# Kernel optimization log

Hardware: AMD Instinct MI355X
Metric: run time of the kernel (lower is better)

Reference implementation:

```python
import jax, jax.numpy as jnp
import numpy as np

DIM = 4096
N_HEADS = 32
N_KV_HEADS = 8
HEAD_DIM = DIM // N_HEADS  # 128
N_REP = N_HEADS // N_KV_HEADS  # 4
THETA = 10000.0
B, S = 4, 1024


def setup_inputs() -> dict:
    key = jax.random.key(0)
    ks = jax.random.split(key, 5)
    sc = 1.0 / np.sqrt(DIM).astype(np.float32)
    x = jax.random.normal(ks[0], (B, S, DIM), jnp.float32)
    wq = jax.random.normal(ks[1], (DIM, N_HEADS * HEAD_DIM), jnp.float32) * sc
    wk = jax.random.normal(ks[2], (DIM, N_KV_HEADS * HEAD_DIM), jnp.float32) * sc
    wv = jax.random.normal(ks[3], (DIM, N_KV_HEADS * HEAD_DIM), jnp.float32) * sc
    wo = jax.random.normal(ks[4], (N_HEADS * HEAD_DIM, DIM), jnp.float32) * sc
    return {"x": x, "wq": wq, "wk": wk, "wv": wv, "wo": wo}


def _rope_cos_sin(seq_len):
    # matches precompute_freqs_cis: freqs over even indices, angles = t * freqs
    freqs = 1.0 / (THETA ** (jnp.arange(0, HEAD_DIM, 2, dtype=jnp.float32) / HEAD_DIM))
    t = jnp.arange(seq_len, dtype=jnp.float32)
    ang = jnp.outer(t, freqs)  # [S, HEAD_DIM//2]
    return jnp.cos(ang), jnp.sin(ang)


def _apply_rope(x, cos, sin):
    # x: [B, S, H, D]; consecutive pairs form complex numbers (view_as_complex)
    xr = x[..., 0::2]
    xi = x[..., 1::2]
    c = cos[None, :, None, :]
    s = sin[None, :, None, :]
    out_r = xr * c - xi * s
    out_i = xr * s + xi * c
    return jnp.stack([out_r, out_i], axis=-1).reshape(x.shape)


def reference(x, wq, wk, wv, wo):
    bsz, seq_len, _ = x.shape
    q = (x @ wq).reshape(bsz, seq_len, N_HEADS, HEAD_DIM)
    k = (x @ wk).reshape(bsz, seq_len, N_KV_HEADS, HEAD_DIM)
    v = (x @ wv).reshape(bsz, seq_len, N_KV_HEADS, HEAD_DIM)
    cos, sin = _rope_cos_sin(seq_len)
    q = _apply_rope(q, cos, sin)
    k = _apply_rope(k, cos, sin)
    # repeat_kv: expand each kv head N_REP times contiguously
    k = jnp.repeat(k, N_REP, axis=2)
    v = jnp.repeat(v, N_REP, axis=2)
    scores = jnp.einsum('bqhd,bkhd->bhqk', q, k) / np.float32(np.sqrt(HEAD_DIM))
    mask = jnp.triu(jnp.full((seq_len, seq_len), -jnp.inf, dtype=scores.dtype), k=1)
    scores = scores + mask
    attn = jax.nn.softmax(scores.astype(jnp.float32), axis=-1).astype(q.dtype)
    out = jnp.einsum('bhqk,bkhd->bqhd', attn, v).reshape(bsz, seq_len, N_HEADS * HEAD_DIM)
    return out @ wo
```

## Files before the change

### kernel.cpp

```cpp
#include <hip/hip_runtime.h>

typedef unsigned short u16;
typedef unsigned int u32;
typedef __attribute__((ext_vector_type(8))) short short8_t;
typedef __attribute__((ext_vector_type(4))) float f32x4;

static constexpr int Bc = 4, Sc = 1024, Hc = 32, HKVc = 8, Dc = 128;
static constexpr int BS = Bc * Sc;
static constexpr int DIMc = 4096;

__device__ __forceinline__ u16 f2bf(float f) {
  u32 u = __float_as_uint(f);
  u32 r = (u + 0x7fffu + ((u >> 16) & 1u)) >> 16;
  return (u16)r;
}
__device__ __forceinline__ float bf2f(u16 u) {
  return __uint_as_float(((u32)u) << 16);
}
__device__ __forceinline__ void gload_lds16(const void* g, void* l) {
  __builtin_amdgcn_global_load_lds((const __attribute__((address_space(1))) void*)g,
                                   (__attribute__((address_space(3))) void*)l, 16, 0, 0);
}

#define SBAR __builtin_amdgcn_sched_barrier(0)
#define PBARRIER do { SBAR; __builtin_amdgcn_s_barrier(); SBAR; } while (0)
#define WAITVM(N) asm volatile("s_waitcnt vmcnt(" #N ")" ::: "memory")

__global__ void rope_table_k(float* __restrict__ tbl) {
  int i = blockIdx.x * 256 + threadIdx.x;
  int s = i >> 6, fi = i & 63;
  float freq = powf(10000.f, -(float)fi / 64.f);
  float ang = (float)s * freq;
  float sv, cv;
  sincosf(ang, &sv, &cv);
  tbl[2 * i] = cv;
  tbl[2 * i + 1] = sv;
}

__global__ void f32_to_bf16_k(const float* __restrict__ in, u16* __restrict__ out, int n4) {
  int i = blockIdx.x * 256 + threadIdx.x;
  if (i >= n4) return;
  float4 v = *(const float4*)(in + (size_t)i * 4);
  uint2 pk;
  pk.x = (u32)f2bf(v.x) | ((u32)f2bf(v.y) << 16);
  pk.y = (u32)f2bf(v.z) | ((u32)f2bf(v.w) << 16);
  *(uint2*)(out + (size_t)i * 4) = pk;
}

__global__ __launch_bounds__(256) void transpose_w_k(const float* __restrict__ W, u16* __restrict__ WT,
                                                     int Kdim, int Ndim) {
  __shared__ float tile[64 * 65];
  const int t = threadIdx.x;
  const int n0 = blockIdx.x * 64, k0 = blockIdx.y * 64;
  #pragma unroll
  for (int p = 0; p < 4; ++p) {
    int idx = p * 256 + t;
    int r = idx >> 4, c = (idx & 15) * 4;
    float4 v = *(const float4*)(W + (size_t)(k0 + r) * Ndim + n0 + c);
    tile[r * 65 + c + 0] = v.x;
    tile[r * 65 + c + 1] = v.y;
    tile[r * 65 + c + 2] = v.z;
    tile[r * 65 + c + 3] = v.w;
  }
  __syncthreads();
  #pragma unroll
  for (int p = 0; p < 2; ++p) {
    int idx = p * 256 + t;
    int n = idx >> 3, c = (idx & 7) * 8;
    alignas(16) u16 o[8];
    #pragma unroll
    for (int i = 0; i < 8; ++i) o[i] = f2bf(tile[(c + i) * 65 + n]);
    *(uint4*)(WT + (size_t)(n0 + n) * Kdim + k0 + c) = *(const uint4*)o;
  }
}

#define MFMAQ(QI)                                                                        \
  do {                                                                                   \
    __builtin_amdgcn_s_setprio(1);                                                       \
    _Pragma("unroll") for (int mf = 0; mf < 4; ++mf)                                     \
      _Pragma("unroll") for (int nf = 0; nf < 2; ++nf)                                   \
        _Pragma("unroll") for (int kk = 0; kk < 2; ++kk)                                 \
          acc[QI][mf][nf] = __builtin_amdgcn_mfma_f32_16x16x32_bf16(                     \
              af[mf][kk], bf[nf][kk], acc[QI][mf][nf], 0, 0, 0);                         \
    __builtin_amdgcn_s_setprio(0);                                                       \
  } while (0)

template <int MODE>
__global__ __launch_bounds__(512, 2) void gemm256(const u16* __restrict__ A, const u16* __restrict__ BT,
                                                  void* __restrict__ Cv, const float* __restrict__ tbl,
                                                  int M, int N, int K) {
  extern __shared__ char smem[];
  const int t = threadIdx.x, l = t & 63, w = t >> 6;
  const int ln15 = l & 15, lh = l >> 4;
  const int NT = K >> 6;

  int id = blockIdx.x;
  int nwg = gridDim.x;
  int swz = ((nwg & 7) == 0) ? ((id & 7) * (nwg >> 3) + (id >> 3)) : id;
  const int nbn = N >> 8;
  const int bm = swz / nbn, bn = swz % nbn;

  const u16* Ag = A + (size_t)bm * 256 * K;
  const u16* Bg = BT + (size_t)bn * 256 * K;

  f32x4 acc[4][4][2];
  #pragma unroll
  for (int q = 0; q < 4; ++q)
    #pragma unroll
    for (int mf = 0; mf < 4; ++mf)
      #pragma unroll
      for (int nf = 0; nf < 2; ++nf) acc[q][mf][nf] = f32x4{0.f, 0.f, 0.f, 0.f};
  short8_t af[4][2], bf[2][2];

  const int srow = (l >> 3);
  const int sck  = (l & 7) ^ srow;
  auto stageA = [&](char* bufbase, int h, int tt) {
    char* lb = bufbase + h * 16384 + w * 1024;
    const u16* g = Ag + (size_t)(h * 128 + w * 8 + srow) * K + tt * 64 + (sck << 3);
    gload_lds16(g, lb);
    gload_lds16(g + (size_t)64 * K, lb + 8192);
  };
  auto stageB = [&](char* bufbase, int h, int tt) {
    char* lb = bufbase + 32768 + h * 16384 + w * 1024;
    const u16* g = Bg + (size_t)(h * 128 + w * 8 + srow) * K + tt * 64 + (sck << 3);
    gload_lds16(g, lb);
    gload_lds16(g + (size_t)64 * K, lb + 8192);
  };
  const int arow = (w >> 2) * 64 + ln15;
  const int brow = (w & 3) * 32 + ln15;
  const int rsw = ln15 & 7;
  auto LDA = [&](const char* cb, int qm) {
    #pragma unroll
    for (int mf = 0; mf < 4; ++mf)
      #pragma unroll
      for (int kk = 0; kk < 2; ++kk)
        af[mf][kk] = *(const short8_t*)(cb + qm * 16384 + (arow + mf * 16) * 128 +
                                        (((kk * 4 + lh) ^ rsw) << 4));
  };
  auto LDB = [&](const char* cb, int qn) {
    #pragma unroll
    for (int nf = 0; nf < 2; ++nf)
      #pragma unroll
      for (int kk = 0; kk < 2; ++kk)
        bf[nf][kk] = *(const short8_t*)(cb + 32768 + qn * 16384 + (brow + nf * 16) * 128 +
                                        (((kk * 4 + lh) ^ rsw) << 4));
  };

  {
    char* b0 = smem;
    char* b1 = smem + 65536;
    stageB(b0, 0, 0);
    stageA(b0, 1, 0);
    stageA(b0, 0, 0);
    stageB(b0, 1, 0);
    stageB(b1, 0, 1);
    stageA(b1, 1, 1);
    stageB(b1, 1, 1);
  }
  WAITVM(6);
  PBARRIER;

  for (int T = 0; T < NT; ++T) {
    char* cb = smem + (T & 1) * 65536;
    char* nb = smem + ((T & 1) ^ 1) * 65536;
    const bool s1 = (T + 1 < NT), s2 = (T + 2 < NT);
    LDA(cb, 0); LDB(cb, 0);
    if (s1) stageA(nb, 0, T + 1);
    MFMAQ(0);
    PBARRIER;
    LDA(cb, 1);
    if (s2) stageB(cb, 0, T + 2);
    MFMAQ(1);
    PBARRIER;
    LDB(cb, 1);
    if (s2) stageA(cb, 1, T + 2);
    MFMAQ(2);
    PBARRIER;
    LDA(cb, 0);
    if (s2) stageB(cb, 1, T + 2);
    MFMAQ(3);
    if (s2)      { WAITVM(6); }
    else if (s1) { WAITVM(0); }
    PBARRIER;
  }

  const int rw = (w >> 2) * 64, cw = (w & 3) * 32;
  #pragma unroll
  for (int qi = 0; qi < 4; ++qi) {
    const int qm = (qi == 1 || qi == 2) ? 1 : 0;
    const int qn = (qi >= 2) ? 1 : 0;
    #pragma unroll
    for (int mf = 0; mf < 4; ++mf)
      #pragma unroll
      for (int nf = 0; nf < 2; ++nf)
        #pragma unroll
        for (int e = 0; e < 4; ++e) {
          int row = bm * 256 + qm * 128 + rw + mf * 16 + lh * 4 + e;
          int col = bn * 256 + qn * 128 + cw + nf * 16 + ln15;
          float v = acc[qi][mf][nf][e];
          if (MODE == 2) {
            float pv = __shfl_xor(v, 1);
            int d = col & 127, hh = col >> 7;
            int s = row & (Sc - 1), bb = row >> 10;
            float2 cs = *(const float2*)(tbl + (size_t)(s * 64 + (d >> 1)) * 2);
            float o = (d & 1) ? (v * cs.x + pv * cs.y) : (v * cs.x - pv * cs.y);
            o *= 0.08838834764831845f;
            ((u16*)Cv)[(((size_t)(bb * Hc + hh) * Sc + s) << 7) + d] = f2bf(o);
          } else {
            size_t idx = (size_t)row * N + col;
            ((float*)Cv)[idx] = v;
          }
        }
  }
}

#define MFMAKV(QM)                                                                       \
  do {                                                                                   \
    __builtin_amdgcn_s_setprio(1);                                                       \
    _Pragma("unroll") for (int mf = 0; mf < 4; ++mf)                                     \
      _Pragma("unroll") for (int nf = 0; nf < 2; ++nf)                                   \
        _Pragma("unroll") for (int kk = 0; kk < 2; ++kk)                                 \
          acc[QM][mf][nf] = __builtin_amdgcn_mfma_f32_16x16x32_bf16(                     \
              af[mf][kk], bf[nf][kk], acc[QM][mf][nf], 0, 0, 0);                         \
    __builtin_amdgcn_s_setprio(0);                                                       \
  } while (0)

__global__ __launch_bounds__(512, 1) void gemm_kv(const u16* __restrict__ A, const u16* __restrict__ BT,
                                                  u16* __restrict__ Krp, u16* __restrict__ Vtp,
                                                  const float* __restrict__ tbl) {
  extern __shared__ char smem[];
  const int t = threadIdx.x, l = t & 63, w = t >> 6;
  const int ln15 = l & 15, lh = l >> 4;
  const int K = 4096, NT = 64;

  int id = blockIdx.x;
  int swz = (id & 7) * 32 + (id >> 3);
  const int bm = swz >> 4, bn = swz & 15;

  const u16* Ag = A + (size_t)bm * 256 * K;
  const u16* Bg = BT + (size_t)bn * 128 * K;

  f32x4 acc[2][4][2];
  #pragma unroll
  for (int q = 0; q < 2; ++q)
    #pragma unroll
    for (int mf = 0; mf < 4; ++mf)
      #pragma unroll
      for (int nf = 0; nf < 2; ++nf) acc[q][mf][nf] = f32x4{0.f, 0.f, 0.f, 0.f};
  short8_t af[4][2], bf[2][2];

  const int srow = (l >> 3);
  const int sck  = (l & 7) ^ srow;
  auto stageA = [&](int buf, int h, int tt) {
    char* lb = smem + buf * 32768 + h * 16384 + w * 2048;
    const u16* g = Ag + (size_t)(h * 128 + w * 16 + srow) * K + tt * 64 + (sck << 3);
    gload_lds16(g, lb);
    gload_lds16(g + (size_t)8 * K, lb + 1024);
  };
  auto stageB = [&](int buf, int tt) {
    char* lb = smem + 65536 + buf * 16384 + w * 2048;
    const u16* g = Bg + (size_t)(w * 16 + srow) * K + tt * 64 + (sck << 3);
    gload_lds16(g, lb);
    gload_lds16(g + (size_t)8 * K, lb + 1024);
  };
  const int arow = (w >> 2) * 64 + ln15;
  const int brow = (w & 3) * 32 + ln15;
  const int rsw = ln15 & 7;
  auto LDA = [&](int buf, int qm) {
    #pragma unroll
    for (int mf = 0; mf < 4; ++mf)
      #pragma unroll
      for (int kk = 0; kk < 2; ++kk)
        af[mf][kk] = *(const short8_t*)(smem + buf * 32768 + qm * 16384 + (arow + mf * 16) * 128 +
                                        (((kk * 4 + lh) ^ rsw) << 4));
  };
  auto LDB = [&](int buf) {
    #pragma unroll
    for (int nf = 0; nf < 2; ++nf)
      #pragma unroll
      for (int kk = 0; kk < 2; ++kk)
        bf[nf][kk] = *(const short8_t*)(smem + 65536 + buf * 16384 + (brow + nf * 16) * 128 +
                                        (((kk * 4 + lh) ^ rsw) << 4));
  };

  stageA(0, 0, 0);
  stageB(0, 0);
  stageA(0, 1, 0);
  WAITVM(2);
  PBARRIER;

  for (int T = 0; T < NT; ++T) {
    const int cb = T & 1, nb = cb ^ 1;
    const bool st = (T + 1 < NT);
    LDA(cb, 0); LDB(cb);
    if (st) stageA(nb, 0, T + 1);
    MFMAKV(0);
    if (st) { WAITVM(2); } else { WAITVM(0); }
    PBARRIER;
    LDA(cb, 1);
    if (st) { stageB(nb, T + 1); stageA(nb, 1, T + 1); }
    MFMAKV(1);
    if (st) { WAITVM(2); }
    PBARRIER;
  }

  #pragma unroll
  for (int qm = 0; qm < 2; ++qm)
    #pragma unroll
    for (int mf = 0; mf < 4; ++mf)
      #pragma unroll
      for (int nf = 0; nf < 2; ++nf)
        #pragma unroll
        for (int e = 0; e < 4; ++e) {
          int row = bm * 256 + qm * 128 + (w >> 2) * 64 + mf * 16 + lh * 4 + e;
          int col = bn * 128 + (w & 3) * 32 + nf * 16 + ln15;
          float v = acc[qm][mf][nf][e];
          float pv = __shfl_xor(v, 1);
          int s = row & (Sc - 1), bb = row >> 10;
          if (col < 1024) {
            int hkv = col >> 7, d = col & 127;
            float2 cs = *(const float2*)(tbl + (size_t)(s * 64 + (d >> 1)) * 2);
            float o = (d & 1) ? (v * cs.x + pv * cs.y) : (v * cs.x - pv * cs.y);
            Krp[(((size_t)(bb * HKVc + hkv) * Sc + s) << 7) + d] = f2bf(o);
          } else {
            int vc = col - 1024;
            int hkv = vc >> 7, d = vc & 127;
            int sl = s & 63;
            int sg = (sl & 32) | (((sl >> 2) & 3) << 3) | (((sl >> 4) & 1) << 2) | (sl & 3);
            Vtp[((size_t)(bb * HKVc + hkv) * Dc + d) * Sc + (s & ~63) + sg] = f2bf(v);
          }
        }
}

__global__ __launch_bounds__(512, 4) void attn_k(const u16* __restrict__ Q, const u16* __restrict__ Kr,
                                                 const u16* __restrict__ Vt, u16* __restrict__ AO) {
  extern __shared__ char smem[];
  const int t = threadIdx.x, l = t & 63, w = t >> 6;
  const int qb = (int)gridDim.x - 1 - (int)blockIdx.x;
  const int h = blockIdx.y, b = blockIdx.z;
  const int hkv = h >> 2;
  const int ln15 = l & 15, lh = l >> 4;
  const int NT = 2 * qb + 2;

  const u16* Kg0 = Kr + (size_t)(b * HKVc + hkv) * Sc * Dc;
  const u16* Vg0 = Vt + (size_t)(b * HKVc + hkv) * Dc * Sc;

  auto stageK = [&](int buf, int tt) {
    char* base = smem + buf * 16384 + w * 2048;
    #pragma unroll
    for (int i = 0; i < 2; ++i) {
      int row = w * 8 + i * 4 + (l >> 4);
      int c = l & 15;
      gload_lds16(Kg0 + (size_t)(tt * 64 + row) * Dc + ((c ^ (row & 7)) << 3), base + i * 1024);
    }
  };
  auto stageV = [&](int buf, int tt) {
    char* base = smem + 32768 + buf * 16384 + w * 2048;
    #pragma unroll
    for (int i = 0; i < 2; ++i) {
      int d = w * 16 + i * 8 + (l >> 3);
      int c = l & 7;
      gload_lds16(Vg0 + (size_t)d * Sc + tt * 64 + ((c ^ (d & 7)) << 3), base + i * 1024);
    }
  };

  short8_t qf[4];
  {
    int q = qb * 128 + w * 16 + ln15;
    const u16* qp = Q + ((size_t)(b * Hc + h) * Sc + q) * Dc + lh * 8;
    #pragma unroll
    for (int ks = 0; ks < 4; ++ks) qf[ks] = *(const short8_t*)(qp + ks * 32);
  }
  SBAR;

  f32x4 oacc[8];
  #pragma unroll
  for (int i = 0; i < 8; ++i) oacc[i] = f32x4{0.f, 0.f, 0.f, 0.f};
  float mrun = -1e30f, lrun = 0.f;

  stageK(0, 0); stageV(0, 0);
  stageK(1, 1); stageV(1, 1);

  const int qmaxw = qb * 128 + w * 16 + 15;
  const int qlane = qb * 128 + w * 16 + ln15;

  for (int T = 0; T < NT; ++T) {
    if (T < NT - 1) { WAITVM(4); } else { WAITVM(0); }
    PBARRIER;
    const char* Kb = smem + (T & 1) * 16384;
    const char* Vb = smem + 32768 + (T & 1) * 16384;

    if (T * 64 <= qmaxw) {
      f32x4 sf[4];
      #pragma unroll
      for (int fc = 0; fc < 4; ++fc) {
        sf[fc] = f32x4{0.f, 0.f, 0.f, 0.f};
        int kvr = fc * 16 + ln15;
        #pragma unroll
        for (int ks = 0; ks < 4; ++ks) {
          int chunk = ks * 4 + lh;
          short8_t kf = *(const short8_t*)(Kb + kvr * 256 + ((chunk ^ (kvr & 7)) << 4));
          sf[fc] = __builtin_amdgcn_mfma_f32_16x16x32_bf16(kf, qf[ks], sf[fc], 0, 0, 0);
        }
      }
      if (T * 64 + 63 > qb * 128 + w * 16) {
        #pragma unroll
        for (int fc = 0; fc < 4; ++fc)
          #pragma unroll
          for (int j = 0; j < 4; ++j) {
            int kvg = T * 64 + fc * 16 + lh * 4 + j;
            if (kvg > qlane) sf[fc][j] = -1e30f;
          }
      }
      float mx = sf[0][0];
      #pragma unroll
      for (int fc = 0; fc < 4; ++fc)
        #pragma unroll
        for (int j = 0; j < 4; ++j) mx = fmaxf(mx, sf[fc][j]);
      mx = fmaxf(mx, __shfl_xor(mx, 16));
      mx = fmaxf(mx, __shfl_xor(mx, 32));
      float mnew = fmaxf(mrun, mx);
      float alpha = __expf(mrun - mnew);
      mrun = mnew;
      float rs = 0.f;
      #pragma unroll
      for (int fc = 0; fc < 4; ++fc)
        #pragma unroll
        for (int j = 0; j < 4; ++j) {
          float p = __expf(sf[fc][j] - mnew);
          sf[fc][j] = p;
          rs += p;
        }
      rs += __shfl_xor(rs, 16);
      rs += __shfl_xor(rs, 32);
      lrun = lrun * alpha + rs;
      float arow[4];
      #pragma unroll
      for (int j = 0; j < 4; ++j) arow[j] = __shfl(alpha, (l & 48) | (lh * 4 + j));
      #pragma unroll
      for (int fd = 0; fd < 8; ++fd)
        #pragma unroll
        for (int j = 0; j < 4; ++j) oacc[fd][j] *= arow[j];
      short8_t pa[2];
      #pragma unroll
      for (int ks = 0; ks < 2; ++ks)
        #pragma unroll
        for (int b2 = 0; b2 < 2; ++b2)
          #pragma unroll
          for (int j = 0; j < 4; ++j) pa[ks][b2 * 4 + j] = (short)f2bf(sf[ks * 2 + b2][j]);
      #pragma unroll
      for (int fd = 0; fd < 8; ++fd) {
        int dcol = fd * 16 + ln15;
        #pragma unroll
        for (int ks = 0; ks < 2; ++ks) {
          int chunk = ks * 4 + lh;
          short8_t vf = *(const short8_t*)(Vb + dcol * 128 + ((chunk ^ (dcol & 7)) << 4));
          oacc[fd] = __builtin_amdgcn_mfma_f32_16x16x32_bf16(pa[ks], vf, oacc[fd], 0, 0, 0);
        }
      }
    }
    PBARRIER;
    if (T + 2 < NT) { stageK(T & 1, T + 2); stageV(T & 1, T + 2); }
  }

  float linv[4];
  #pragma unroll
  for (int j = 0; j < 4; ++j) linv[j] = 1.f / __shfl(lrun, (l & 48) | (lh * 4 + j));
  #pragma unroll
  for (int j = 0; j < 4; ++j) {
    int q = qb * 128 + w * 16 + lh * 4 + j;
    u16* op = AO + (size_t)(b * Sc + q) * DIMc + h * Dc + ln15;
    #pragma unroll
    for (int fd = 0; fd < 8; ++fd) op[fd * 16] = f2bf(oacc[fd][j] * linv[j]);
  }
}

extern "C" void kernel_launch(void* const* d_in, const int* in_sizes, int n_in,
                              void* d_out, int out_size, void* d_ws, size_t ws_size,
                              hipStream_t stream) {
  const float* x  = (const float*)d_in[0];
  const float* wq = (const float*)d_in[1];
  const float* wk = (const float*)d_in[2];
  const float* wv = (const float*)d_in[3];
  const float* wo = (const float*)d_in[4];
  float* out = (float*)d_out;

  char* ws = (char*)d_ws;
  size_t off = 0;
  auto alloc = [&](size_t bytes) -> char* {
    char* p = ws + off;
    off += (bytes + 255) & ~(size_t)255;
    return p;
  };
  float* tbl  = (float*)alloc((size_t)Sc * 64 * 2 * 4);
  u16* xb    = (u16*)alloc((size_t)BS * DIMc * 2);
  u16* wqT   = (u16*)alloc((size_t)4096 * 4096 * 2);
  u16* wkvT  = (u16*)alloc((size_t)2048 * 4096 * 2);
  u16* Qb    = (u16*)alloc((size_t)BS * 4096 * 2);
  u16* Krp   = (u16*)alloc((size_t)BS * 1024 * 2);
  u16* Vtp   = (u16*)alloc((size_t)BS * 1024 * 2);
  u16* AO = xb;
  u16* woT = wqT;

  rope_table_k<<<(Sc * 64) / 256, 256, 0, stream>>>(tbl);
  f32_to_bf16_k<<<(BS * DIMc / 4) / 256, 256, 0, stream>>>(x, xb, BS * DIMc / 4);

  transpose_w_k<<<dim3(64, 64), 256, 0, stream>>>(wq, wqT, 4096, 4096);
  gemm256<2><<<256, 512, 131072, stream>>>(xb, wqT, Qb, tbl, 4096, 4096, 4096);

  transpose_w_k<<<dim3(16, 64), 256, 0, stream>>>(wk, wkvT, 4096, 1024);
  transpose_w_k<<<dim3(16, 64), 256, 0, stream>>>(wv, wkvT + (size_t)1024 * 4096, 4096, 1024);
  gemm_kv<<<256, 512, 98304, stream>>>(xb, wkvT, Krp, Vtp, tbl);

  attn_k<<<dim3(8, Hc, Bc), 512, 65536, stream>>>(Qb, Krp, Vtp, AO);

  transpose_w_k<<<dim3(64, 64), 256, 0, stream>>>(wo, woT, 4096, 4096);
  gemm256<1><<<256, 512, 131072, stream>>>(AO, woT, out, tbl, 4096, 4096, 4096);
}
```

Measured before the change: 487.1 us.

## Restructure GEMM main loops to single barrier per tile with B fragments held in registers

The 256x256 GEMM and the KV GEMM main loops are reorganised. Each k-tile now has one barrier instead of four or two. B fragments for both halves are kept in registers and preloaded for the next tile, and A fragments use two register sets so MFMAs can run back to back. Staging now fills the whole other buffer for tile T+1 rather than interleaving prefetches two tiles ahead. This cuts barrier and LDS-wait overhead, but it adds register pressure and uses full vmcnt(0) waits, which shortens the prefetch distance.

```diff
diff --git a/kernel.cpp b/kernel.cpp
--- a/kernel.cpp
+++ b/kernel.cpp
@@ -74,14 +74,14 @@
   }
 }
 
-#define MFMAQ(QI)                                                                        \
+#define MFMAQ(QI, AF, BF)                                                                \
   do {                                                                                   \
     __builtin_amdgcn_s_setprio(1);                                                       \
     _Pragma("unroll") for (int mf = 0; mf < 4; ++mf)                                     \
       _Pragma("unroll") for (int nf = 0; nf < 2; ++nf)                                   \
         _Pragma("unroll") for (int kk = 0; kk < 2; ++kk)                                 \
           acc[QI][mf][nf] = __builtin_amdgcn_mfma_f32_16x16x32_bf16(                     \
-              af[mf][kk], bf[nf][kk], acc[QI][mf][nf], 0, 0, 0);                         \
+              AF[mf][kk], BF[nf][kk], acc[QI][mf][nf], 0, 0, 0);                         \
     __builtin_amdgcn_s_setprio(0);                                                       \
   } while (0)
 
@@ -110,7 +110,7 @@
     for (int mf = 0; mf < 4; ++mf)
       #pragma unroll
       for (int nf = 0; nf < 2; ++nf) acc[q][mf][nf] = f32x4{0.f, 0.f, 0.f, 0.f};
-  short8_t af[4][2], bf[2][2];
+  short8_t af[4][2], af2[4][2], bfB0[2][2], bfB1[2][2];
 
   const int srow = (l >> 3);
   const int sck  = (l & 7) ^ srow;
@@ -129,59 +129,47 @@
   const int arow = (w >> 2) * 64 + ln15;
   const int brow = (w & 3) * 32 + ln15;
   const int rsw = ln15 & 7;
-  auto LDA = [&](const char* cb, int qm) {
+  auto LDA = [&](const char* cb, int qm, short8_t (&dst)[4][2]) {
     #pragma unroll
     for (int mf = 0; mf < 4; ++mf)
       #pragma unroll
       for (int kk = 0; kk < 2; ++kk)
-        af[mf][kk] = *(const short8_t*)(cb + qm * 16384 + (arow + mf * 16) * 128 +
-                                        (((kk * 4 + lh) ^ rsw) << 4));
-  };
-  auto LDB = [&](const char* cb, int qn) {
+        dst[mf][kk] = *(const short8_t*)(cb + qm * 16384 + (arow + mf * 16) * 128 +
+                                         (((kk * 4 + lh) ^ rsw) << 4));
+  };
+  auto LDB = [&](const char* cb, int qn, short8_t (&dst)[2][2]) {
     #pragma unroll
     for (int nf = 0; nf < 2; ++nf)
       #pragma unroll
       for (int kk = 0; kk < 2; ++kk)
-        bf[nf][kk] = *(const short8_t*)(cb + 32768 + qn * 16384 + (brow + nf * 16) * 128 +
-                                        (((kk * 4 + lh) ^ rsw) << 4));
-  };
-
-  {
-    char* b0 = smem;
-    char* b1 = smem + 65536;
-    stageB(b0, 0, 0);
-    stageA(b0, 1, 0);
-    stageA(b0, 0, 0);
-    stageB(b0, 1, 0);
-    stageB(b1, 0, 1);
-    stageA(b1, 1, 1);
-    stageB(b1, 1, 1);
-  }
-  WAITVM(6);
+        dst[nf][kk] = *(const short8_t*)(cb + 32768 + qn * 16384 + (brow + nf * 16) * 128 +
+                                         (((kk * 4 + lh) ^ rsw) << 4));
+  };
+
+  stageA(smem, 0, 0);
+  stageB(smem, 0, 0);
+  stageA(smem, 1, 0);
+  stageB(smem, 1, 0);
+  WAITVM(0);
   PBARRIER;
+  LDB(smem, 0, bfB0);
+  LDB(smem, 1, bfB1);
 
   for (int T = 0; T < NT; ++T) {
     char* cb = smem + (T & 1) * 65536;
     char* nb = smem + ((T & 1) ^ 1) * 65536;
-    const bool s1 = (T + 1 < NT), s2 = (T + 2 < NT);
-    LDA(cb, 0); LDB(cb, 0);
-    if (s1) stageA(nb, 0, T + 1);
-    MFMAQ(0);
+    const bool s1 = (T + 1 < NT);
+    if (s1) { stageA(nb, 0, T + 1); stageB(nb, 0, T + 1); }
+    LDA(cb, 0, af);
+    MFMAQ(0, af, bfB0);
+    MFMAQ(3, af, bfB1);
+    if (s1) { stageA(nb, 1, T + 1); stageB(nb, 1, T + 1); }
+    LDA(cb, 1, af2);
+    MFMAQ(1, af2, bfB0);
+    MFMAQ(2, af2, bfB1);
+    WAITVM(0);
     PBARRIER;
-    LDA(cb, 1);
-    if (s2) stageB(cb, 0, T + 2);
-    MFMAQ(1);
-    PBARRIER;
-    LDB(cb, 1);
-    if (s2) stageA(cb, 1, T + 2);
-    MFMAQ(2);
-    PBARRIER;
-    LDA(cb, 0);
-    if (s2) stageB(cb, 1, T + 2);
-    MFMAQ(3);
-    if (s2)      { WAITVM(6); }
-    else if (s1) { WAITVM(0); }
-    PBARRIER;
+    if (s1) { LDB(nb, 0, bfB0); LDB(nb, 1, bfB1); }
   }
 
   const int rw = (w >> 2) * 64, cw = (w & 3) * 32;
@@ -214,14 +202,14 @@
   }
 }
 
-#define MFMAKV(QM)                                                                       \
+#define MFMAKV(QM, AF)                                                                   \
   do {                                                                                   \
     __builtin_amdgcn_s_setprio(1);                                                       \
     _Pragma("unroll") for (int mf = 0; mf < 4; ++mf)                                     \
       _Pragma("unroll") for (int nf = 0; nf < 2; ++nf)                                   \
         _Pragma("unroll") for (int kk = 0; kk < 2; ++kk)                                 \
           acc[QM][mf][nf] = __builtin_amdgcn_mfma_f32_16x16x32_bf16(                     \
-              af[mf][kk], bf[nf][kk], acc[QM][mf][nf], 0, 0, 0);                         \
+              AF[mf][kk], bf[nf][kk], acc[QM][mf][nf], 0, 0, 0);                         \
     __builtin_amdgcn_s_setprio(0);                                                       \
   } while (0)
 
@@ -247,7 +235,7 @@
     for (int mf = 0; mf < 4; ++mf)
       #pragma unroll
       for (int nf = 0; nf < 2; ++nf) acc[q][mf][nf] = f32x4{0.f, 0.f, 0.f, 0.f};
-  short8_t af[4][2], bf[2][2];
+  short8_t af[4][2], af2[4][2], bf[2][2];
 
   const int srow = (l >> 3);
   const int sck  = (l & 7) ^ srow;
@@ -266,13 +254,13 @@
   const int arow = (w >> 2) * 64 + ln15;
   const int brow = (w & 3) * 32 + ln15;
   const int rsw = ln15 & 7;
-  auto LDA = [&](int buf, int qm) {
+  auto LDA = [&](int buf, int qm, short8_t (&dst)[4][2]) {
     #pragma unroll
     for (int mf = 0; mf < 4; ++mf)
       #pragma unroll
       for (int kk = 0; kk < 2; ++kk)
-        af[mf][kk] = *(const short8_t*)(smem + buf * 32768 + qm * 16384 + (arow + mf * 16) * 128 +
-                                        (((kk * 4 + lh) ^ rsw) << 4));
+        dst[mf][kk] = *(const short8_t*)(smem + buf * 32768 + qm * 16384 + (arow + mf * 16) * 128 +
+                                         (((kk * 4 + lh) ^ rsw) << 4));
   };
   auto LDB = [&](int buf) {
     #pragma unroll
@@ -286,22 +274,22 @@
   stageA(0, 0, 0);
   stageB(0, 0);
   stageA(0, 1, 0);
-  WAITVM(2);
+  WAITVM(0);
   PBARRIER;
+  LDB(0);
 
   for (int T = 0; T < NT; ++T) {
     const int cb = T & 1, nb = cb ^ 1;
     const bool st = (T + 1 < NT);
-    LDA(cb, 0); LDB(cb);
-    if (st) stageA(nb, 0, T + 1);
-    MFMAKV(0);
-    if (st) { WAITVM(2); } else { WAITVM(0); }
+    if (st) { stageA(nb, 0, T + 1); stageB(nb, T + 1); }
+    LDA(cb, 0, af);
+    MFMAKV(0, af);
+    if (st) stageA(nb, 1, T + 1);
+    LDA(cb, 1, af2);
+    MFMAKV(1, af2);
+    WAITVM(0);
     PBARRIER;
-    LDA(cb, 1);
-    if (st) { stageB(nb, T + 1); stageA(nb, 1, T + 1); }
-    MFMAKV(1);
-    if (st) { WAITVM(2); }
-    PBARRIER;
+    if (st) LDB(nb);
   }
 
   #pragma unroll
```

New measurement: 477.5 us. 2.0% less time.
